# Kernel tuning notes

Hardware: AMD Instinct MI355X
Metric: run time of the kernel (lower is better)

## Reference

```python
import jax, jax.numpy as jnp
import numpy as np

EPS = 1e-5
NEG_SLOPE = 0.1


def _gcn_layer(x, row, col, W, b):
    # GCNConv, improved=True (self-loop weight 2.0), symmetric normalization.
    N = x.shape[0]
    xw = x @ W                                   # [N, H]
    ew = jnp.ones(row.shape[0], dtype=x.dtype)   # edge_weight=None -> ones
    deg = jax.ops.segment_sum(ew, col, num_segments=N) + 2.0  # +2 from improved self loop
    dinv = jax.lax.rsqrt(deg)                    # deg >= 2, always finite
    norm = dinv[row] * dinv[col]                 # [E]
    agg = jax.ops.segment_sum(norm[:, None] * xw[row], col, num_segments=N)
    agg = agg + (2.0 * dinv * dinv)[:, None] * xw  # self-loop contribution
    return agg + b


def _batchnorm(x, w, b):
    # training-mode BN over node dim (biased variance), eps=1e-5
    mu = jnp.mean(x, axis=0)
    var = jnp.mean((x - mu) ** 2, axis=0)
    return (x - mu) * jax.lax.rsqrt(var + EPS) * w + b


def setup_inputs() -> dict:
    key = jax.random.key(0)
    ks = jax.random.split(key, 10)
    N, E, F, H, OUT, G = 100000, 800000, 128, 128, 128, 2048
    x = jax.random.normal(ks[0], (N, F), dtype=jnp.float32)
    edge_index = jax.random.randint(ks[1], (2, E), 0, N, dtype=jnp.int64)
    batch = jnp.sort(jax.random.randint(ks[2], (N,), 0, G, dtype=jnp.int64))
    s1 = 1.0 / np.sqrt(F)
    s2 = 1.0 / np.sqrt(H)
    return {
        "x": x,
        "edge_index": edge_index,
        "batch": batch,
        "W1": jax.random.uniform(ks[3], (F, H), jnp.float32, -s1, s1),
        "b1": jnp.zeros((H,), jnp.float32),
        "bn1_w": jnp.ones((H,), jnp.float32),
        "bn1_b": jnp.zeros((H,), jnp.float32),
        "W2": jax.random.uniform(ks[4], (H, H), jnp.float32, -s2, s2),
        "b2": jnp.zeros((H,), jnp.float32),
        "bn2_w": jnp.ones((H,), jnp.float32),
        "bn2_b": jnp.zeros((H,), jnp.float32),
        "Wf": jax.random.uniform(ks[5], (H, OUT), jnp.float32, -s2, s2),
        "bf": jax.random.uniform(ks[6], (OUT,), jnp.float32, -s2, s2),
        "num_graphs": G,
    }


def reference(x, edge_index, batch, W1, b1, bn1_w, bn1_b, W2, b2, bn2_w, bn2_b, Wf, bf, num_graphs):
    row, col = edge_index[0], edge_index[1]
    h = _gcn_layer(x, row, col, W1, b1)
    h = jax.nn.leaky_relu(_batchnorm(h, bn1_w, bn1_b), NEG_SLOPE)
    # dropout omitted (deterministic reference / eval mode)
    h = _gcn_layer(h, row, col, W2, b2)
    h = jax.nn.leaky_relu(_batchnorm(h, bn2_w, bn2_b), NEG_SLOPE)
    pooled = jax.ops.segment_max(h, batch, num_segments=num_graphs)  # [G, H]
    pooled = jnp.where(jnp.isneginf(pooled), 0.0, pooled)            # empty graphs -> 0
    return pooled @ Wf + bf
```

## Files before the change

kernel.cpp:

```cpp
#include <hip/hip_runtime.h>
#include <hip/hip_bf16.h>

#define EPSV 1e-5f
#define SLOPE 0.1f

typedef __attribute__((ext_vector_type(8))) unsigned short ushort8v;

static __device__ inline unsigned short f2bf(float f) {
    __hip_bfloat16 b = __float2bfloat16(f);
    return *reinterpret_cast<unsigned short*>(&b);
}
static __device__ inline float bf2f(unsigned short u) {
    return __uint_as_float(((unsigned)u) << 16);
}

__global__ __launch_bounds__(256) void k_count(const int* __restrict__ col,
                                               unsigned* __restrict__ cnt, int E) {
    int e = blockIdx.x * 256 + threadIdx.x;
    if (e < E) atomicAdd(&cnt[col[e]], 1u);
}

__global__ __launch_bounds__(256) void k_dinv(const unsigned* __restrict__ cnt,
                                              float* __restrict__ dinv, int N) {
    int n = blockIdx.x * 256 + threadIdx.x;
    if (n < N) dinv[n] = rsqrtf((float)cnt[n] + 2.0f);
}

__global__ __launch_bounds__(256) void k_chunk_sum(const unsigned* __restrict__ cnt, int N,
                                                   unsigned* __restrict__ bsum) {
    __shared__ unsigned ls[256];
    int base = blockIdx.x * 1024;
    unsigned s = 0;
    for (int i = threadIdx.x; i < 1024; i += 256) {
        int idx = base + i;
        if (idx < N) s += cnt[idx];
    }
    ls[threadIdx.x] = s;
    __syncthreads();
    for (int st = 128; st > 0; st >>= 1) {
        if (threadIdx.x < st) ls[threadIdx.x] += ls[threadIdx.x + st];
        __syncthreads();
    }
    if (threadIdx.x == 0) bsum[blockIdx.x] = ls[0];
}

__global__ void k_scan_bsum(unsigned* __restrict__ bsum, int nb) {
    if (threadIdx.x == 0 && blockIdx.x == 0) {
        unsigned acc = 0;
        for (int i = 0; i < nb; i++) { unsigned v = bsum[i]; bsum[i] = acc; acc += v; }
    }
}

__global__ __launch_bounds__(256) void k_scan_chunks(const unsigned* __restrict__ cnt, int N,
                                                     const unsigned* __restrict__ bsum,
                                                     int* __restrict__ off, int E) {
    __shared__ unsigned ls[256];
    int base = blockIdx.x * 1024;
    unsigned v[4];
    unsigned s = 0;
#pragma unroll
    for (int j = 0; j < 4; j++) {
        int idx = base + threadIdx.x * 4 + j;
        v[j] = (idx < N) ? cnt[idx] : 0u;
        s += v[j];
    }
    ls[threadIdx.x] = s;
    __syncthreads();
    if (threadIdx.x == 0) {
        unsigned acc = bsum[blockIdx.x];
        for (int i = 0; i < 256; i++) { unsigned t = ls[i]; ls[i] = acc; acc += t; }
    }
    __syncthreads();
    unsigned acc = ls[threadIdx.x];
#pragma unroll
    for (int j = 0; j < 4; j++) {
        int idx = base + threadIdx.x * 4 + j;
        if (idx < N) off[idx] = (int)acc;
        acc += v[j];
    }
    if (base + threadIdx.x * 4 <= N - 1 && N - 1 < base + threadIdx.x * 4 + 4) off[N] = E;
}

__global__ __launch_bounds__(256) void k_place(const int* __restrict__ row,
                                               const int* __restrict__ col,
                                               const float* __restrict__ dinv,
                                               int* __restrict__ cursor,
                                               int2* __restrict__ spack, int E) {
    int e = blockIdx.x * 256 + threadIdx.x;
    if (e >= E) return;
    int r = row[e], c = col[e];
    int pos = atomicAdd(&cursor[c], 1);
    spack[pos] = make_int2(r, __float_as_int(dinv[r] * dinv[c]));
}

template <int MODE>
__global__ __launch_bounds__(256) void k_gemm_t(const float* __restrict__ X,
                                                const float* __restrict__ W,
                                                const float* __restrict__ sums, float invN,
                                                const float* __restrict__ bnw,
                                                const float* __restrict__ bnb,
                                                const float* __restrict__ bias,
                                                void* __restrict__ Yv, int N) {
    __shared__ float xs[64][132];
    __shared__ float sc[128], sb[128];
    const int tid = threadIdx.x;
    if (MODE == 1) {
        if (tid < 128) {
            float mu = sums[tid] * invN;
            float var = sums[128 + tid] * invN - mu * mu;
            float s = rsqrtf(var + EPSV) * bnw[tid];
            sc[tid] = s;
            sb[tid] = bnb[tid] - mu * s;
        }
        __syncthreads();
    }
    const int base = blockIdx.x * 64;
    for (int i = tid; i < 2048; i += 256) {
        int r = i >> 5, c4 = i & 31;
        int row = base + r; if (row >= N) row = N - 1;
        float4 v = ((const float4*)(X + (size_t)row * 128))[c4];
        if (MODE == 1) {
            int f = c4 * 4;
            v.x = fmaf(v.x, sc[f + 0], sb[f + 0]); v.x = v.x > 0.f ? v.x : SLOPE * v.x;
            v.y = fmaf(v.y, sc[f + 1], sb[f + 1]); v.y = v.y > 0.f ? v.y : SLOPE * v.y;
            v.z = fmaf(v.z, sc[f + 2], sb[f + 2]); v.z = v.z > 0.f ? v.z : SLOPE * v.z;
            v.w = fmaf(v.w, sc[f + 3], sb[f + 3]); v.w = v.w > 0.f ? v.w : SLOPE * v.w;
        }
        *(float4*)(&xs[r][c4 * 4]) = v;
    }
    __syncthreads();
    const int c0 = (tid & 31) * 4;
    const int rg = tid >> 5;
    float acc[8][4];
#pragma unroll
    for (int i = 0; i < 8; i++) { acc[i][0] = acc[i][1] = acc[i][2] = acc[i][3] = 0.f; }
    for (int k = 0; k < 128; k += 4) {
        float4 w0 = *(const float4*)(W + (size_t)(k + 0) * 128 + c0);
        float4 w1 = *(const float4*)(W + (size_t)(k + 1) * 128 + c0);
        float4 w2 = *(const float4*)(W + (size_t)(k + 2) * 128 + c0);
        float4 w3 = *(const float4*)(W + (size_t)(k + 3) * 128 + c0);
#pragma unroll
        for (int i = 0; i < 8; i++) {
            float4 a = *(const float4*)(&xs[rg + 8 * i][k]);
            acc[i][0] = fmaf(a.x, w0.x, fmaf(a.y, w1.x, fmaf(a.z, w2.x, fmaf(a.w, w3.x, acc[i][0]))));
            acc[i][1] = fmaf(a.x, w0.y, fmaf(a.y, w1.y, fmaf(a.z, w2.y, fmaf(a.w, w3.y, acc[i][1]))));
            acc[i][2] = fmaf(a.x, w0.z, fmaf(a.y, w1.z, fmaf(a.z, w2.z, fmaf(a.w, w3.z, acc[i][2]))));
            acc[i][3] = fmaf(a.x, w0.w, fmaf(a.y, w1.w, fmaf(a.z, w2.w, fmaf(a.w, w3.w, acc[i][3]))));
        }
    }
#pragma unroll
    for (int i = 0; i < 8; i++) {
        int row = base + rg + 8 * i;
        if (row < N) {
            if (MODE == 2) {
                float4 o = make_float4(acc[i][0] + bias[c0], acc[i][1] + bias[c0 + 1],
                                       acc[i][2] + bias[c0 + 2], acc[i][3] + bias[c0 + 3]);
                ((float4*)((float*)Yv + (size_t)row * 128))[tid & 31] = o;
            } else {
                ushort4 o;
                o.x = f2bf(acc[i][0]); o.y = f2bf(acc[i][1]);
                o.z = f2bf(acc[i][2]); o.w = f2bf(acc[i][3]);
                ((ushort4*)((unsigned short*)Yv + (size_t)row * 128))[tid & 31] = o;
            }
        }
    }
}

__global__ __launch_bounds__(256) void k_agg5(const unsigned short* __restrict__ xwh,
                                              const int* __restrict__ off,
                                              const int2* __restrict__ spack,
                                              const float* __restrict__ dinv,
                                              const float* __restrict__ bias,
                                              float* __restrict__ h,
                                              float* __restrict__ sums, int N) {
    __shared__ float ls1[128], ls2[128];
    const int tid = threadIdx.x;
    if (tid < 128) { ls1[tid] = 0.f; ls2[tid] = 0.f; }
    __syncthreads();

    const int q = tid & 15;
    const int grp = (blockIdx.x * 256 + tid) >> 4;
    const int nGrp = gridDim.x * 16;

    float bj[8];
#pragma unroll
    for (int j = 0; j < 8; j++) bj[j] = bias[q * 8 + j];
    float st1[8] = {0, 0, 0, 0, 0, 0, 0, 0};
    float st2[8] = {0, 0, 0, 0, 0, 0, 0, 0};

    for (int n = grp; n < N; n += nGrp) {
        const int s = off[n], e = off[n + 1];
        float a[8] = {0, 0, 0, 0, 0, 0, 0, 0};
        int i = s;
        for (; i + 8 <= e; i += 8) {
            int2 p0 = spack[i + 0], p1 = spack[i + 1], p2 = spack[i + 2], p3 = spack[i + 3];
            int2 p4 = spack[i + 4], p5 = spack[i + 5], p6 = spack[i + 6], p7 = spack[i + 7];
            ushort8v v0 = *(const ushort8v*)(xwh + (size_t)p0.x * 128 + q * 8);
            ushort8v v1 = *(const ushort8v*)(xwh + (size_t)p1.x * 128 + q * 8);
            ushort8v v2 = *(const ushort8v*)(xwh + (size_t)p2.x * 128 + q * 8);
            ushort8v v3 = *(const ushort8v*)(xwh + (size_t)p3.x * 128 + q * 8);
            ushort8v v4 = *(const ushort8v*)(xwh + (size_t)p4.x * 128 + q * 8);
            ushort8v v5 = *(const ushort8v*)(xwh + (size_t)p5.x * 128 + q * 8);
            ushort8v v6 = *(const ushort8v*)(xwh + (size_t)p6.x * 128 + q * 8);
            ushort8v v7 = *(const ushort8v*)(xwh + (size_t)p7.x * 128 + q * 8);
            float n0 = __int_as_float(p0.y), n1 = __int_as_float(p1.y);
            float n2 = __int_as_float(p2.y), n3 = __int_as_float(p3.y);
            float n4 = __int_as_float(p4.y), n5 = __int_as_float(p5.y);
            float n6 = __int_as_float(p6.y), n7 = __int_as_float(p7.y);
#pragma unroll
            for (int j = 0; j < 8; j++) {
                float t = fmaf(n0, bf2f(v0[j]), fmaf(n1, bf2f(v1[j]),
                          fmaf(n2, bf2f(v2[j]), n3 * bf2f(v3[j]))));
                float u = fmaf(n4, bf2f(v4[j]), fmaf(n5, bf2f(v5[j]),
                          fmaf(n6, bf2f(v6[j]), n7 * bf2f(v7[j]))));
                a[j] += t + u;
            }
        }
        for (; i + 4 <= e; i += 4) {
            int2 p0 = spack[i + 0], p1 = spack[i + 1], p2 = spack[i + 2], p3 = spack[i + 3];
            ushort8v v0 = *(const ushort8v*)(xwh + (size_t)p0.x * 128 + q * 8);
            ushort8v v1 = *(const ushort8v*)(xwh + (size_t)p1.x * 128 + q * 8);
            ushort8v v2 = *(const ushort8v*)(xwh + (size_t)p2.x * 128 + q * 8);
            ushort8v v3 = *(const ushort8v*)(xwh + (size_t)p3.x * 128 + q * 8);
            float n0 = __int_as_float(p0.y), n1 = __int_as_float(p1.y);
            float n2 = __int_as_float(p2.y), n3 = __int_as_float(p3.y);
#pragma unroll
            for (int j = 0; j < 8; j++) {
                a[j] += fmaf(n0, bf2f(v0[j]), fmaf(n1, bf2f(v1[j]),
                        fmaf(n2, bf2f(v2[j]), n3 * bf2f(v3[j]))));
            }
        }
        for (; i < e; ++i) {
            int2 p = spack[i];
            ushort8v v = *(const ushort8v*)(xwh + (size_t)p.x * 128 + q * 8);
            float nm = __int_as_float(p.y);
#pragma unroll
            for (int j = 0; j < 8; j++) a[j] = fmaf(nm, bf2f(v[j]), a[j]);
        }
        float dc = dinv[n];
        float sl = 2.f * dc * dc;
        ushort8v xv = *(const ushort8v*)(xwh + (size_t)n * 128 + q * 8);
        float o[8];
#pragma unroll
        for (int j = 0; j < 8; j++) {
            o[j] = fmaf(sl, bf2f(xv[j]), a[j]) + bj[j];
            st1[j] += o[j];
            st2[j] += o[j] * o[j];
        }
        float4* hp = (float4*)(h + (size_t)n * 128 + q * 8);
        hp[0] = make_float4(o[0], o[1], o[2], o[3]);
        hp[1] = make_float4(o[4], o[5], o[6], o[7]);
    }
#pragma unroll
    for (int j = 0; j < 8; j++) {
        atomicAdd(&ls1[q * 8 + j], st1[j]);
        atomicAdd(&ls2[q * 8 + j], st2[j]);
    }
    __syncthreads();
    if (tid < 128) {
        atomicAdd(&sums[tid], ls1[tid]);
        atomicAdd(&sums[128 + tid], ls2[tid]);
    }
}

__global__ __launch_bounds__(256) void k_pool_init(unsigned* __restrict__ p, int total) {
    int i = blockIdx.x * 256 + threadIdx.x;
    if (i < total) p[i] = 0x007FFFFFu;
}

__device__ inline unsigned enc_f(float x) {
    unsigned u = __float_as_uint(x);
    return (u & 0x80000000u) ? ~u : (u | 0x80000000u);
}

__global__ __launch_bounds__(256) void k_pool2(const float* __restrict__ h,
                                               const int* __restrict__ batch,
                                               const float* __restrict__ sums, float invN,
                                               const float* __restrict__ bnw,
                                               const float* __restrict__ bnb,
                                               unsigned* __restrict__ pooled, int N) {
    const int f = threadIdx.x & 127;
    const int half = threadIdx.x >> 7;
    float mu = sums[f] * invN;
    float var = sums[128 + f] * invN - mu * mu;
    float scale = rsqrtf(var + EPSV) * bnw[f];
    float bias = bnb[f] - mu * scale;
    const int base = blockIdx.x * 128;
    const int end = min(base + 128, N);
    float m = -__builtin_inff();
    int g = -1;
    for (int n = base + half; n < end; n += 2) {
        int bg = batch[n];
        if (bg != g) {
            if (g >= 0) atomicMax(&pooled[(size_t)g * 128 + f], enc_f(m));
            g = bg;
            m = -__builtin_inff();
        }
        float v = fmaf(h[(size_t)n * 128 + f], scale, bias);
        v = v > 0.f ? v : SLOPE * v;
        m = fmaxf(m, v);
    }
    if (g >= 0) atomicMax(&pooled[(size_t)g * 128 + f], enc_f(m));
}

__global__ __launch_bounds__(256) void k_decode(unsigned* __restrict__ p, int total) {
    int i = blockIdx.x * 256 + threadIdx.x;
    if (i >= total) return;
    unsigned u = p[i];
    float v;
    if (u == 0x007FFFFFu) v = 0.f;
    else if (u & 0x80000000u) v = __uint_as_float(u & 0x7FFFFFFFu);
    else v = __uint_as_float(~u);
    p[i] = __float_as_uint(v);
}

extern "C" void kernel_launch(void* const* d_in, const int* in_sizes, int n_in,
                              void* d_out, int out_size, void* d_ws, size_t ws_size,
                              hipStream_t stream) {
    const float* x     = (const float*)d_in[0];
    const int*   ei    = (const int*)d_in[1];
    const int*   batch = (const int*)d_in[2];
    const float* W1    = (const float*)d_in[3];
    const float* b1    = (const float*)d_in[4];
    const float* bn1w  = (const float*)d_in[5];
    const float* bn1b  = (const float*)d_in[6];
    const float* W2    = (const float*)d_in[7];
    const float* b2    = (const float*)d_in[8];
    const float* bn2w  = (const float*)d_in[9];
    const float* bn2b  = (const float*)d_in[10];
    const float* Wf    = (const float*)d_in[11];
    const float* bf    = (const float*)d_in[12];

    const int N = in_sizes[0] / 128;
    const int E = in_sizes[1] / 2;
    const int G = out_size / 128;
    const int* rowp = ei;
    const int* colp = ei + E;
    float* out = (float*)d_out;
    const float invN = 1.0f / N;

    char* w = (char*)d_ws;
    unsigned short* bufAh = (unsigned short*)w; w += (size_t)N * 128 * 2;
    float*    bufB   = (float*)w;    w += (size_t)N * 128 * 4;
    float*    dinv   = (float*)w;    w += (size_t)N * 4;
    unsigned* cnt    = (unsigned*)w; w += (size_t)N * 4;
    int*      off    = (int*)w;      w += (size_t)(N + 4) * 4;
    unsigned* bsum   = (unsigned*)w; w += 1024 * 4;
    int2*     spack  = (int2*)w;     w += (size_t)E * 8;
    float*    sums   = (float*)w;    w += 512 * 4;
    unsigned* pooled = (unsigned*)w; w += (size_t)G * 128 * 4;

    float* sums1 = sums;
    float* sums2 = sums + 256;
    const int nb = (N + 1023) / 1024;

    hipMemsetAsync(cnt, 0, (size_t)N * 4, stream);
    hipMemsetAsync(sums, 0, 512 * 4, stream);
    k_count<<<(E + 255) / 256, 256, 0, stream>>>(colp, cnt, E);
    k_dinv<<<(N + 255) / 256, 256, 0, stream>>>(cnt, dinv, N);
    k_chunk_sum<<<nb, 256, 0, stream>>>(cnt, N, bsum);
    k_scan_bsum<<<1, 64, 0, stream>>>(bsum, nb);
    k_scan_chunks<<<nb, 256, 0, stream>>>(cnt, N, bsum, off, E);
    hipMemcpyAsync(cnt, off, (size_t)N * 4, hipMemcpyDeviceToDevice, stream);
    k_place<<<(E + 255) / 256, 256, 0, stream>>>(rowp, colp, dinv, (int*)cnt, spack, E);

    const int aggBlocks = 2048;

    k_gemm_t<0><<<(N + 63) / 64, 256, 0, stream>>>(x, W1, nullptr, 0.f, nullptr, nullptr,
                                                   nullptr, bufAh, N);
    k_agg5<<<aggBlocks, 256, 0, stream>>>(bufAh, off, spack, dinv, b1, bufB, sums1, N);

    k_gemm_t<1><<<(N + 63) / 64, 256, 0, stream>>>(bufB, W2, sums1, invN, bn1w, bn1b,
                                                   nullptr, bufAh, N);
    k_agg5<<<aggBlocks, 256, 0, stream>>>(bufAh, off, spack, dinv, b2, bufB, sums2, N);

    k_pool_init<<<(G * 128 + 255) / 256, 256, 0, stream>>>(pooled, G * 128);
    k_pool2<<<(N + 127) / 128, 256, 0, stream>>>(bufB, batch, sums2, invN, bn2w, bn2b,
                                                 pooled, N);
    k_decode<<<(G * 128 + 255) / 256, 256, 0, stream>>>(pooled, G * 128);

    k_gemm_t<2><<<(G + 63) / 64, 256, 0, stream>>>((const float*)pooled, Wf, nullptr, 0.f,
                                                   nullptr, nullptr, bf, out, G);
}
```

Measured before the change: 497.2 us.

## Use bf16 MFMA for dense GEMMs with pre-transposed bf16 weights

Replaces the scalar FP32 FMA GEMM with a bf16 MFMA 16x16x32 kernel. Activations are staged in shared memory as bf16, and the weights are transposed and converted to bf16 by a new prep kernel. The goal is to cut ALU time in the three dense matmuls, at the cost of lower input precision, including the final FP32 output GEMM. The aggregation grid size also doubles, from 2048 to 4096 blocks.

```diff
diff --git a/kernel.cpp b/kernel.cpp
--- a/kernel.cpp
+++ b/kernel.cpp
@@ -5,6 +5,8 @@
 #define SLOPE 0.1f
 
 typedef __attribute__((ext_vector_type(8))) unsigned short ushort8v;
+typedef __attribute__((ext_vector_type(8))) short bf16x8;
+typedef __attribute__((ext_vector_type(4))) float f32x4;
 
 static __device__ inline unsigned short f2bf(float f) {
     __hip_bfloat16 b = __float2bfloat16(f);
@@ -93,15 +95,31 @@
     spack[pos] = make_int2(r, __float_as_int(dinv[r] * dinv[c]));
 }
 
+__global__ __launch_bounds__(256) void k_prepw(const float* __restrict__ W1,
+                                               const float* __restrict__ W2,
+                                               const float* __restrict__ Wf,
+                                               unsigned short* __restrict__ wT) {
+    int m = blockIdx.x >> 4;
+    int idx = (blockIdx.x & 15) * 256 + threadIdx.x;
+    const float* W = (m == 0) ? W1 : (m == 1) ? W2 : Wf;
+    unsigned short* T = wT + (size_t)m * 16384;
+    int k = idx >> 5, n4 = (idx & 31) * 4;
+    float4 v = *(const float4*)(W + (size_t)k * 128 + n4);
+    T[(size_t)(n4 + 0) * 128 + k] = f2bf(v.x);
+    T[(size_t)(n4 + 1) * 128 + k] = f2bf(v.y);
+    T[(size_t)(n4 + 2) * 128 + k] = f2bf(v.z);
+    T[(size_t)(n4 + 3) * 128 + k] = f2bf(v.w);
+}
+
 template <int MODE>
-__global__ __launch_bounds__(256) void k_gemm_t(const float* __restrict__ X,
-                                                const float* __restrict__ W,
+__global__ __launch_bounds__(256) void k_gemm_m(const float* __restrict__ X,
+                                                const unsigned short* __restrict__ wT,
                                                 const float* __restrict__ sums, float invN,
                                                 const float* __restrict__ bnw,
                                                 const float* __restrict__ bnb,
                                                 const float* __restrict__ bias,
                                                 void* __restrict__ Yv, int N) {
-    __shared__ float xs[64][132];
+    __shared__ unsigned short xs[64][136];
     __shared__ float sc[128], sb[128];
     const int tid = threadIdx.x;
     if (MODE == 1) {
@@ -126,41 +144,42 @@
             v.z = fmaf(v.z, sc[f + 2], sb[f + 2]); v.z = v.z > 0.f ? v.z : SLOPE * v.z;
             v.w = fmaf(v.w, sc[f + 3], sb[f + 3]); v.w = v.w > 0.f ? v.w : SLOPE * v.w;
         }
-        *(float4*)(&xs[r][c4 * 4]) = v;
-    }
-    __syncthreads();
-    const int c0 = (tid & 31) * 4;
-    const int rg = tid >> 5;
-    float acc[8][4];
-#pragma unroll
-    for (int i = 0; i < 8; i++) { acc[i][0] = acc[i][1] = acc[i][2] = acc[i][3] = 0.f; }
-    for (int k = 0; k < 128; k += 4) {
-        float4 w0 = *(const float4*)(W + (size_t)(k + 0) * 128 + c0);
-        float4 w1 = *(const float4*)(W + (size_t)(k + 1) * 128 + c0);
-        float4 w2 = *(const float4*)(W + (size_t)(k + 2) * 128 + c0);
-        float4 w3 = *(const float4*)(W + (size_t)(k + 3) * 128 + c0);
-#pragma unroll
-        for (int i = 0; i < 8; i++) {
-            float4 a = *(const float4*)(&xs[rg + 8 * i][k]);
-            acc[i][0] = fmaf(a.x, w0.x, fmaf(a.y, w1.x, fmaf(a.z, w2.x, fmaf(a.w, w3.x, acc[i][0]))));
-            acc[i][1] = fmaf(a.x, w0.y, fmaf(a.y, w1.y, fmaf(a.z, w2.y, fmaf(a.w, w3.y, acc[i][1]))));
-            acc[i][2] = fmaf(a.x, w0.z, fmaf(a.y, w1.z, fmaf(a.z, w2.z, fmaf(a.w, w3.z, acc[i][2]))));
-            acc[i][3] = fmaf(a.x, w0.w, fmaf(a.y, w1.w, fmaf(a.z, w2.w, fmaf(a.w, w3.w, acc[i][3]))));
-        }
-    }
-#pragma unroll
-    for (int i = 0; i < 8; i++) {
-        int row = base + rg + 8 * i;
-        if (row < N) {
-            if (MODE == 2) {
-                float4 o = make_float4(acc[i][0] + bias[c0], acc[i][1] + bias[c0 + 1],
-                                       acc[i][2] + bias[c0 + 2], acc[i][3] + bias[c0 + 3]);
-                ((float4*)((float*)Yv + (size_t)row * 128))[tid & 31] = o;
-            } else {
-                ushort4 o;
-                o.x = f2bf(acc[i][0]); o.y = f2bf(acc[i][1]);
-                o.z = f2bf(acc[i][2]); o.w = f2bf(acc[i][3]);
-                ((ushort4*)((unsigned short*)Yv + (size_t)row * 128))[tid & 31] = o;
+        ushort4 o;
+        o.x = f2bf(v.x); o.y = f2bf(v.y); o.z = f2bf(v.z); o.w = f2bf(v.w);
+        *(ushort4*)(&xs[r][c4 * 4]) = o;
+    }
+    __syncthreads();
+
+    const int lane = tid & 63;
+    const int m0 = (tid >> 6) * 16;
+    const int mr = lane & 15;
+    const int kg = lane >> 4;
+    f32x4 acc[8];
+#pragma unroll
+    for (int nf = 0; nf < 8; nf++) acc[nf] = (f32x4){0.f, 0.f, 0.f, 0.f};
+
+#pragma unroll
+    for (int kt = 0; kt < 4; kt++) {
+        bf16x8 a = *(const bf16x8*)(&xs[m0 + mr][kt * 32 + kg * 8]);
+#pragma unroll
+        for (int nf = 0; nf < 8; nf++) {
+            bf16x8 b = *(const bf16x8*)(wT + (size_t)(nf * 16 + mr) * 128 + kt * 32 + kg * 8);
+            acc[nf] = __builtin_amdgcn_mfma_f32_16x16x32_bf16(a, b, acc[nf], 0, 0, 0);
+        }
+    }
+
+#pragma unroll
+    for (int nf = 0; nf < 8; nf++) {
+#pragma unroll
+        for (int r = 0; r < 4; r++) {
+            int row = base + m0 + kg * 4 + r;
+            if (row < N) {
+                int coln = nf * 16 + mr;
+                if (MODE == 2) {
+                    ((float*)Yv)[(size_t)row * 128 + coln] = acc[nf][r] + bias[coln];
+                } else {
+                    ((unsigned short*)Yv)[(size_t)row * 128 + coln] = f2bf(acc[nf][r]);
+                }
             }
         }
     }
@@ -349,6 +368,7 @@
     int2*     spack  = (int2*)w;     w += (size_t)E * 8;
     float*    sums   = (float*)w;    w += 512 * 4;
     unsigned* pooled = (unsigned*)w; w += (size_t)G * 128 * 4;
+    unsigned short* wT = (unsigned short*)w; w += 3 * 16384 * 2;
 
     float* sums1 = sums;
     float* sums2 = sums + 256;
@@ -356,6 +376,7 @@
 
     hipMemsetAsync(cnt, 0, (size_t)N * 4, stream);
     hipMemsetAsync(sums, 0, 512 * 4, stream);
+    k_prepw<<<48, 256, 0, stream>>>(W1, W2, Wf, wT);
     k_count<<<(E + 255) / 256, 256, 0, stream>>>(colp, cnt, E);
     k_dinv<<<(N + 255) / 256, 256, 0, stream>>>(cnt, dinv, N);
     k_chunk_sum<<<nb, 256, 0, stream>>>(cnt, N, bsum);
@@ -364,14 +385,15 @@
     hipMemcpyAsync(cnt, off, (size_t)N * 4, hipMemcpyDeviceToDevice, stream);
     k_place<<<(E + 255) / 256, 256, 0, stream>>>(rowp, colp, dinv, (int*)cnt, spack, E);
 
-    const int aggBlocks = 2048;
-
-    k_gemm_t<0><<<(N + 63) / 64, 256, 0, stream>>>(x, W1, nullptr, 0.f, nullptr, nullptr,
-                                                   nullptr, bufAh, N);
+    const int aggBlocks = 4096;
+    const int gemmGrid = (N + 63) / 64;
+
+    k_gemm_m<0><<<gemmGrid, 256, 0, stream>>>(x, wT, nullptr, 0.f, nullptr, nullptr,
+                                              nullptr, bufAh, N);
     k_agg5<<<aggBlocks, 256, 0, stream>>>(bufAh, off, spack, dinv, b1, bufB, sums1, N);
 
-    k_gemm_t<1><<<(N + 63) / 64, 256, 0, stream>>>(bufB, W2, sums1, invN, bn1w, bn1b,
-                                                   nullptr, bufAh, N);
+    k_gemm_m<1><<<gemmGrid, 256, 0, stream>>>(bufB, wT + 16384, sums1, invN, bn1w, bn1b,
+                                              nullptr, bufAh, N);
     k_agg5<<<aggBlocks, 256, 0, stream>>>(bufAh, off, spack, dinv, b2, bufB, sums2, N);
 
     k_pool_init<<<(G * 128 + 255) / 256, 256, 0, stream>>>(pooled, G * 128);
@@ -379,6 +401,7 @@
                                                  pooled, N);
     k_decode<<<(G * 128 + 255) / 256, 256, 0, stream>>>(pooled, G * 128);
 
-    k_gemm_t<2><<<(G + 63) / 64, 256, 0, stream>>>((const float*)pooled, Wf, nullptr, 0.f,
-                                                   nullptr, nullptr, bf, out, G);
-}
+    k_gemm_m<2><<<(G + 63) / 64, 256, 0, stream>>>((const float*)pooled, wT + 32768,
+                                                   nullptr, 0.f, nullptr, nullptr, bf,
+                                                   out, G);
+}
```

Result: slower. 606.4 us (+22.0%).
